# Kernel optimization log

Hardware: AMD Instinct MI355X
Metric: run time of the kernel (lower is better)

## Reference

```python
import jax, jax.numpy as jnp
import numpy as np


def _integral(x):
    # x: [C, H, W] -> summed-area table [C, H+1, W+1] with zero first row/col
    s = jnp.cumsum(jnp.cumsum(x, axis=-2), axis=-1)
    return jnp.pad(s, ((0, 0), (1, 0), (1, 0)))


def _box_sums(S, x0, y0, x1, y1):
    # S: [C, H+1, W+1]; boxes half-open [y0:y1, x0:x1] -> sums [C, N]
    return S[:, y1, x1] - S[:, y0, x1] - S[:, y1, x0] + S[:, y0, x0]


def setup_inputs() -> dict:
    key = jax.random.key(0)
    C, H, W, K, N = 256, 512, 512, 21, 2560
    k1, k2, k3, k4, k5, k6, k7 = jax.random.split(key, 7)
    feature_map = jax.random.normal(k1, (C, H, W), dtype=jnp.float32)
    norm_cam_bg = jax.random.uniform(k2, (K, H, W), dtype=jnp.float32)
    # valid crop boxes (xmin, ymin, xmax, ymax) with 8..64 px extent
    x0 = jax.random.randint(k3, (N,), 0, W - 64)
    y0 = jax.random.randint(k4, (N,), 0, H - 64)
    bw = jax.random.randint(k5, (N,), 8, 64)
    bh = jax.random.randint(k6, (N,), 8, 64)
    boxes = jnp.stack([x0, y0, x0 + bw, y0 + bh], axis=1).astype(jnp.int32)
    labels = jax.random.randint(k7, (N,), 0, K).astype(jnp.int32)
    return {"feature_map": feature_map, "norm_cam_bg": norm_cam_bg,
            "boxes": boxes, "labels": labels}


def reference(feature_map, norm_cam_bg, boxes, labels):
    # feature_map: [C, H, W]; norm_cam_bg: [K, H, W]; boxes: [N, 4] int; labels: [N] int
    K = norm_cam_bg.shape[0]
    N = boxes.shape[0]
    x0, y0, x1, y1 = boxes[:, 0], boxes[:, 1], boxes[:, 2], boxes[:, 3]
    area = ((x1 - x0) * (y1 - y0)).astype(feature_map.dtype)  # [N]

    # per-box adaptive_avg_pool2d(region, (1,1)) == mean over region, via integral image
    S = _integral(feature_map)                                # [C, H+1, W+1]
    pool = _box_sums(S, x0, y0, x1, y1).T / area[:, None]     # [N, C]

    # foreground score: fraction of pixels in box where argmax(CAM) == region label
    cam_predict = jnp.argmax(norm_cam_bg, axis=0)             # [H, W]
    onehot = jax.nn.one_hot(cam_predict, K, dtype=feature_map.dtype)  # [H, W, K]
    Sm = _integral(jnp.moveaxis(onehot, -1, 0))               # [K, H+1, W+1]
    fg_sums = _box_sums(Sm, x0, y0, x1, y1)                   # [K, N]
    fg_score = fg_sums[labels, jnp.arange(N)] / area          # [N]

    return pool, fg_score
```

## Files before the change

kernel.cpp:

```cpp
#include <hip/hip_runtime.h>

#define HWD (512*512)
#define Wd 512
#define Hd 512
#define Cd 256
#define Kd 21
#define Nd 2560
#define NSTRIP 4
#define SROWS 128

__device__ __forceinline__ float dpp_scan_incl(float x) {
    int xi, t;
    xi = __float_as_int(x);
    t = __builtin_amdgcn_update_dpp(0, xi, 0x111, 0xf, 0xf, true);
    x += __int_as_float(t);
    xi = __float_as_int(x);
    t = __builtin_amdgcn_update_dpp(0, xi, 0x112, 0xf, 0xf, true);
    x += __int_as_float(t);
    xi = __float_as_int(x);
    t = __builtin_amdgcn_update_dpp(0, xi, 0x114, 0xf, 0xf, true);
    x += __int_as_float(t);
    xi = __float_as_int(x);
    t = __builtin_amdgcn_update_dpp(0, xi, 0x118, 0xf, 0xf, true);
    x += __int_as_float(t);
    xi = __float_as_int(x);
    t = __builtin_amdgcn_update_dpp(0, xi, 0x142, 0xa, 0xf, false);
    x += __int_as_float(t);
    xi = __float_as_int(x);
    t = __builtin_amdgcn_update_dpp(0, xi, 0x143, 0xc, 0xf, false);
    x += __int_as_float(t);
    return x;
}

__global__ __launch_bounds__(512) void k_pre(const float* __restrict__ ncb,
                                             const int* __restrict__ boxes,
                                             unsigned char* __restrict__ map,
                                             int* __restrict__ ev_start,
                                             unsigned int* __restrict__ ev_list) {
    const int t = threadIdx.x;
    if (blockIdx.x < 512) {
        const int p = blockIdx.x * 512 + t;
        float best = ncb[p];
        int bi = 0;
        #pragma unroll
        for (int k = 1; k < Kd; ++k) {
            float v = ncb[(size_t)k * HWD + p];
            if (v > best) { best = v; bi = k; }
        }
        map[p] = (unsigned char)bi;
        return;
    }

    __shared__ int cnt[512];
    __shared__ int cur[512];
    __shared__ int tt[8];
    const int lane = t & 63, wv = t >> 6;
    cnt[t] = 0;
    __syncthreads();
    for (int n = t; n < Nd; n += 512) {
        const int y0 = boxes[n * 4 + 1];
        const int y1 = boxes[n * 4 + 3];
        if (y0 > 0) atomicAdd(&cnt[y0 - 1], 1);
        atomicAdd(&cnt[y1 - 1], 1);
    }
    __syncthreads();
    const int v = cnt[t];
    int inc = v;
    #pragma unroll
    for (int d = 1; d < 64; d <<= 1) {
        int u = __shfl_up(inc, d);
        if (lane >= d) inc += u;
    }
    if (lane == 63) tt[wv] = inc;
    __syncthreads();
    int off = 0;
    #pragma unroll
    for (int w = 0; w < 8; ++w) if (w < wv) off += tt[w];
    inc += off;
    cur[t] = inc - v;
    ev_start[t] = inc - v;
    if (t == 511) ev_start[512] = inc;
    __syncthreads();
    for (int n = t; n < Nd; n += 512) {
        const int y0 = boxes[n * 4 + 1];
        const int y1 = boxes[n * 4 + 3];
        if (y0 > 0) {
            const int r = y0 - 1;
            const int p = atomicAdd(&cur[r], 1);
            ev_list[p] = (unsigned)n | ((unsigned)r << 12) | 0x80000000u;
        }
        const int r = y1 - 1;
        const int p = atomicAdd(&cur[r], 1);
        ev_list[p] = (unsigned)n | ((unsigned)r << 12);
    }
}

__global__ __launch_bounds__(512) void k_ipool(const float* __restrict__ f,
                                               const int* __restrict__ boxes,
                                               const int* __restrict__ ev_start,
                                               const unsigned int* __restrict__ ev_list,
                                               float* __restrict__ pool_acc) {
    const int c     = blockIdx.x >> 2;
    const int strip = blockIdx.x & 3;
    const int t = threadIdx.x;
    const int lane = t & 63, wv = t >> 6;
    const float* F = f + (size_t)c * HWD + (size_t)(strip * SROWS) * Wd;

    __shared__ float S[8][512];
    __shared__ float partial[Nd];

    for (int n = t; n < Nd; n += 512) partial[n] = 0.f;

    float colacc = 0.f;

    const float* rp0 = F + (size_t)wv * Wd + lane * 8;
    float4 a0 = *(const float4*)(rp0);
    float4 b0 = *(const float4*)(rp0 + 4);
    const float* rp1 = F + (size_t)(8 + wv) * Wd + lane * 8;
    float4 a1 = *(const float4*)(rp1);
    float4 b1 = *(const float4*)(rp1 + 4);

    for (int yb = 0; yb < SROWS; yb += 8) {
        const bool more2 = (yb + 16 < SROWS);
        float4 na, nb;
        if (more2) {
            const float* np = F + (size_t)(yb + 16 + wv) * Wd + lane * 8;
            na = *(const float4*)(np);
            nb = *(const float4*)(np + 4);
        }

        float v0 = a0.x, v1 = v0 + a0.y, v2 = v1 + a0.z, v3 = v2 + a0.w;
        float v4 = v3 + b0.x, v5 = v4 + b0.y, v6 = v5 + b0.z, v7 = v6 + b0.w;
        const float xx = dpp_scan_incl(v7);
        const float off = xx - v7;
        float4 o0 = { v0 + off, v1 + off, v2 + off, v3 + off };
        float4 o1 = { v4 + off, v5 + off, v6 + off, v7 + off };
        *(float4*)&S[wv][lane * 8]     = o0;
        *(float4*)&S[wv][lane * 8 + 4] = o1;
        __syncthreads();

        float sv[8];
        #pragma unroll
        for (int j = 0; j < 8; ++j) sv[j] = S[j][t];
        #pragma unroll
        for (int j = 0; j < 8; ++j) {
            colacc += sv[j];
            S[j][t] = colacc;
        }
        __syncthreads();

        const int g0 = strip * SROWS + yb;
        const int e0 = ev_start[g0];
        const int e1 = ev_start[g0 + 8];
        for (int e = e0 + t; e < e1; e += 512) {
            const unsigned ev = ev_list[e];
            const int n  = ev & 0xFFF;
            const int rr = (ev >> 12) & 7;
            const int x0 = boxes[n * 4 + 0];
            const int x1 = boxes[n * 4 + 2];
            const float sx1 = S[rr][x1 - 1];
            const float sx0 = (x0 > 0) ? S[rr][x0 - 1] : 0.f;
            const float d = sx1 - sx0;
            partial[n] += (ev & 0x80000000u) ? -d : d;
        }
        __syncthreads();

        a0 = a1; b0 = b1;
        if (more2) { a1 = na; b1 = nb; }
    }

    S[0][t] = colacc;
    __syncthreads();
    for (int n = t; n < Nd; n += 512) {
        const int x0 = boxes[n * 4 + 0];
        const int y0 = boxes[n * 4 + 1];
        const int x1 = boxes[n * 4 + 2];
        const int y1 = boxes[n * 4 + 3];
        float p = partial[n];
        const float tdiff = S[0][x1 - 1] - ((x0 > 0) ? S[0][x0 - 1] : 0.f);
        if (strip < ((y1 - 1) >> 7)) p += tdiff;
        if (y0 > 0 && strip < ((y0 - 1) >> 7)) p -= tdiff;
        pool_acc[((size_t)(strip * Cd + c)) * Nd + n] = p;
    }
}

__global__ __launch_bounds__(512) void k_pool2(const float* __restrict__ pool_acc,
                                               const int* __restrict__ boxes,
                                               float* __restrict__ pool) {
    __shared__ float P[32][257];
    __shared__ float rarea[32];
    const int t = threadIdx.x;
    const int n0 = blockIdx.x * 32;

    if (t < 32) {
        const int x0 = boxes[(n0 + t) * 4 + 0];
        const int y0 = boxes[(n0 + t) * 4 + 1];
        const int x1 = boxes[(n0 + t) * 4 + 2];
        const int y1 = boxes[(n0 + t) * 4 + 3];
        rarea[t] = 1.f / (float)((x1 - x0) * (y1 - y0));
    }

    const int ni = t & 31, ci = t >> 5;
    #pragma unroll
    for (int co = 0; co < 16; ++co) {
        const int c = co * 16 + ci;
        float v = 0.f;
        #pragma unroll
        for (int s = 0; s < NSTRIP; ++s)
            v += pool_acc[((size_t)(s * Cd + c)) * Nd + n0 + ni];
        P[ni][c] = v;
    }
    __syncthreads();

    const int c = t & 255, nn = t >> 8;
    #pragma unroll
    for (int no = 0; no < 16; ++no) {
        const int i = no * 2 + nn;
        pool[(size_t)(n0 + i) * Cd + c] = P[i][c] * rarea[i];
    }
}

__global__ __launch_bounds__(256) void k_fg(const unsigned char* __restrict__ map,
                                            const int* __restrict__ boxes,
                                            const int* __restrict__ labels,
                                            float* __restrict__ fg) {
    const int n = blockIdx.x;
    const int x0 = boxes[n * 4 + 0];
    const int y0 = boxes[n * 4 + 1];
    const int x1 = boxes[n * 4 + 2];
    const int y1 = boxes[n * 4 + 3];
    const int lab = labels[n];
    const int lane = threadIdx.x & 63;
    const int wv   = threadIdx.x >> 6;
    const int w = x1 - x0;

    int cnt = 0;
    for (int yy = y0 + wv; yy < y1; yy += 4) {
        if (lane < w)
            cnt += (map[yy * Wd + x0 + lane] == lab) ? 1 : 0;
    }
    #pragma unroll
    for (int d = 32; d; d >>= 1) cnt += __shfl_down(cnt, d);

    __shared__ int sred[4];
    if (lane == 0) sred[wv] = cnt;
    __syncthreads();
    if (threadIdx.x == 0) {
        int tot = sred[0] + sred[1] + sred[2] + sred[3];
        float area = (float)(w * (y1 - y0));
        fg[n] = (float)tot / area;
    }
}

extern "C" void kernel_launch(void* const* d_in, const int* in_sizes, int n_in,
                              void* d_out, int out_size, void* d_ws, size_t ws_size,
                              hipStream_t stream) {
    (void)in_sizes; (void)n_in; (void)out_size; (void)ws_size;

    const float* feature_map = (const float*)d_in[0];
    const float* norm_cam_bg = (const float*)d_in[1];
    const int*   boxes       = (const int*)d_in[2];
    const int*   labels      = (const int*)d_in[3];

    float* out_pool = (float*)d_out;
    float* out_fg   = out_pool + (size_t)Nd * Cd;

    char* ws = (char*)d_ws;
    unsigned char* map      = (unsigned char*)ws;
    int*           ev_start = (int*)(ws + 262144);
    unsigned int*  ev_list  = (unsigned int*)(ws + 266240);
    float*         pool_acc = (float*)(ws + 286720);

    k_pre<<<513, 512, 0, stream>>>(norm_cam_bg, boxes, map, ev_start, ev_list);
    k_ipool<<<Cd * NSTRIP, 512, 0, stream>>>(feature_map, boxes, ev_start, ev_list,
                                             pool_acc);
    k_pool2<<<Nd / 32, 512, 0, stream>>>(pool_acc, boxes, out_pool);
    k_fg<<<Nd, 256, 0, stream>>>(map, boxes, labels, out_fg);
}
```

Measured before the change: 79.32 us.

## Move CAM argmax into pool reduction kernel and use nontemporal feature loads

The per-pixel CAM argmax blocks move out of the first kernel and into the pool-reduction kernel as extra blocks. The first kernel becomes a single-block event builder, so the heavy feature-map integral pass starts sooner and the argmax work shares a launch with the small pool2 reduction. Feature-map and CAM loads switch to nontemporal loads to reduce cache pollution on single-use streaming data. The extra argmax blocks may lengthen the pool2 launch and delay the fg kernel that depends on the map.

```diff
diff --git a/kernel.cpp b/kernel.cpp
--- a/kernel.cpp
+++ b/kernel.cpp
@@ -9,6 +9,8 @@
 #define NSTRIP 4
 #define SROWS 128
 
+typedef float vf4 __attribute__((ext_vector_type(4)));
+
 __device__ __forceinline__ float dpp_scan_incl(float x) {
     int xi, t;
     xi = __float_as_int(x);
@@ -32,25 +34,10 @@
     return x;
 }
 
-__global__ __launch_bounds__(512) void k_pre(const float* __restrict__ ncb,
-                                             const int* __restrict__ boxes,
-                                             unsigned char* __restrict__ map,
-                                             int* __restrict__ ev_start,
-                                             unsigned int* __restrict__ ev_list) {
+__global__ __launch_bounds__(512) void k_events(const int* __restrict__ boxes,
+                                                int* __restrict__ ev_start,
+                                                unsigned int* __restrict__ ev_list) {
     const int t = threadIdx.x;
-    if (blockIdx.x < 512) {
-        const int p = blockIdx.x * 512 + t;
-        float best = ncb[p];
-        int bi = 0;
-        #pragma unroll
-        for (int k = 1; k < Kd; ++k) {
-            float v = ncb[(size_t)k * HWD + p];
-            if (v > best) { best = v; bi = k; }
-        }
-        map[p] = (unsigned char)bi;
-        return;
-    }
-
     __shared__ int cnt[512];
     __shared__ int cur[512];
     __shared__ int tt[8];
@@ -114,19 +101,19 @@
     float colacc = 0.f;
 
     const float* rp0 = F + (size_t)wv * Wd + lane * 8;
-    float4 a0 = *(const float4*)(rp0);
-    float4 b0 = *(const float4*)(rp0 + 4);
+    vf4 a0 = __builtin_nontemporal_load((const vf4*)(rp0));
+    vf4 b0 = __builtin_nontemporal_load((const vf4*)(rp0 + 4));
     const float* rp1 = F + (size_t)(8 + wv) * Wd + lane * 8;
-    float4 a1 = *(const float4*)(rp1);
-    float4 b1 = *(const float4*)(rp1 + 4);
+    vf4 a1 = __builtin_nontemporal_load((const vf4*)(rp1));
+    vf4 b1 = __builtin_nontemporal_load((const vf4*)(rp1 + 4));
 
     for (int yb = 0; yb < SROWS; yb += 8) {
         const bool more2 = (yb + 16 < SROWS);
-        float4 na, nb;
+        vf4 na, nb;
         if (more2) {
             const float* np = F + (size_t)(yb + 16 + wv) * Wd + lane * 8;
-            na = *(const float4*)(np);
-            nb = *(const float4*)(np + 4);
+            na = __builtin_nontemporal_load((const vf4*)(np));
+            nb = __builtin_nontemporal_load((const vf4*)(np + 4));
         }
 
         float v0 = a0.x, v1 = v0 + a0.y, v2 = v1 + a0.z, v3 = v2 + a0.w;
@@ -184,13 +171,30 @@
     }
 }
 
-__global__ __launch_bounds__(512) void k_pool2(const float* __restrict__ pool_acc,
-                                               const int* __restrict__ boxes,
-                                               float* __restrict__ pool) {
+__global__ __launch_bounds__(512) void k_pool2a(const float* __restrict__ pool_acc,
+                                                const float* __restrict__ ncb,
+                                                const int* __restrict__ boxes,
+                                                float* __restrict__ pool,
+                                                unsigned char* __restrict__ map) {
+    const int bid = blockIdx.x;
+    const int t = threadIdx.x;
+
+    if (bid >= Nd / 32) {
+        const int p = (bid - Nd / 32) * 512 + t;
+        float best = __builtin_nontemporal_load(ncb + p);
+        int bi = 0;
+        #pragma unroll
+        for (int k = 1; k < Kd; ++k) {
+            float v = __builtin_nontemporal_load(ncb + (size_t)k * HWD + p);
+            if (v > best) { best = v; bi = k; }
+        }
+        map[p] = (unsigned char)bi;
+        return;
+    }
+
     __shared__ float P[32][257];
     __shared__ float rarea[32];
-    const int t = threadIdx.x;
-    const int n0 = blockIdx.x * 32;
+    const int n0 = bid * 32;
 
     if (t < 32) {
         const int x0 = boxes[(n0 + t) * 4 + 0];
@@ -271,9 +275,10 @@
     unsigned int*  ev_list  = (unsigned int*)(ws + 266240);
     float*         pool_acc = (float*)(ws + 286720);
 
-    k_pre<<<513, 512, 0, stream>>>(norm_cam_bg, boxes, map, ev_start, ev_list);
+    k_events<<<1, 512, 0, stream>>>(boxes, ev_start, ev_list);
     k_ipool<<<Cd * NSTRIP, 512, 0, stream>>>(feature_map, boxes, ev_start, ev_list,
                                              pool_acc);
-    k_pool2<<<Nd / 32, 512, 0, stream>>>(pool_acc, boxes, out_pool);
+    k_pool2a<<<Nd / 32 + 512, 512, 0, stream>>>(pool_acc, norm_cam_bg, boxes,
+                                                out_pool, map);
     k_fg<<<Nd, 256, 0, stream>>>(map, boxes, labels, out_fg);
 }
```

New measurement: 89.85 us. 13.3% more time.
